# Optimization experiments

Measured on AMD Instinct MI355X. Metric: run time of the kernel, lower is better.

Reference implementation:

```python
import jax, jax.numpy as jnp
import numpy as np

FACTOR = 1.0

def _dct_matrix():
    n = 8
    D = np.zeros((n * n, n * n), dtype=np.float32)
    for u in range(n):
        for v in range(n):
            au = 1.0 / np.sqrt(2.0) if u == 0 else 1.0
            av = 1.0 / np.sqrt(2.0) if v == 0 else 1.0
            alpha = au * av * 0.25
            for x in range(n):
                for y in range(n):
                    D[u * n + v, x * n + y] = alpha * np.cos((2 * x + 1) * u * np.pi / 16) * np.cos((2 * y + 1) * v * np.pi / 16)
    return D

def _y_quant_table():
    t = np.array([[16, 11, 10, 16, 24, 40, 51, 61], [12, 12, 14, 19, 26, 58, 60, 55],
                  [14, 13, 16, 24, 40, 57, 69, 56], [14, 17, 22, 29, 51, 87, 80, 62],
                  [18, 22, 37, 56, 68, 109, 103, 77], [24, 35, 55, 64, 81, 104, 113, 92],
                  [49, 64, 78, 87, 103, 121, 120, 101], [72, 92, 95, 98, 112, 100, 103, 99]],
                 dtype=np.float32).T
    return t

def _c_quant_table():
    t = np.full((8, 8), 99, dtype=np.float32)
    t[:4, :4] = np.array([[17, 18, 24, 47], [18, 21, 26, 66], [24, 26, 56, 99], [47, 66, 99, 99]],
                          dtype=np.float32).T
    return t

_D = jnp.asarray(_dct_matrix())          # [64,64]
_QT = jnp.stack([jnp.asarray(_y_quant_table()),
                 jnp.asarray(_c_quant_table()),
                 jnp.asarray(_c_quant_table())], axis=0) * FACTOR  # [3,8,8]

def setup_inputs() -> dict:
    key = jax.random.key(0)
    image = jax.random.uniform(key, (32, 3, 512, 512), dtype=jnp.float32)
    return {"image": image}

def _diffjpeg(image):
    x = jnp.clip(image, 0.0, 1.0)
    B, C, H, W = x.shape  # H, W multiples of 8 -> no padding branch
    r, g, b = x[:, 0], x[:, 1], x[:, 2]
    y = 0.299 * r + 0.587 * g + 0.114 * b
    cb = (b - y) * 0.564 + 0.5
    cr = (r - y) * 0.713 + 0.5
    ycbcr = jnp.stack([y, cb, cr], axis=1)  # [B,3,H,W]
    # blockify into 8x8 tiles
    nh, nw = H // 8, W // 8
    blocks = ycbcr.reshape(B, C, nh, 8, nw, 8).transpose(0, 1, 2, 4, 3, 5)  # [B,C,nh,nw,8,8]
    flat = blocks.reshape(-1, 64) * 255.0 - 128.0
    dct = flat @ _D.T                      # matmul(D, flat.T).T
    dctb = dct.reshape(B, C, nh, nw, 8, 8)
    qte = _QT[None, :, None, None, :, :]   # [1,3,1,1,8,8]
    q = dctb / qte
    q = q + jax.lax.stop_gradient(jnp.round(q) - q)  # STE rounding
    deq = q * qte
    idct = deq.reshape(-1, 64) @ _D        # matmul(D.T, x.T).T
    idct = (idct + 128.0) / 255.0
    img = idct.reshape(B, C, nh, nw, 8, 8).transpose(0, 1, 2, 4, 3, 5).reshape(B, C, H, W)
    yy, ycb, ycr = img[:, 0], img[:, 1] - 0.5, img[:, 2] - 0.5
    rr = yy + 1.403 * ycr
    gg = yy - 0.714 * ycr - 0.344 * ycb
    bb = yy + 1.773 * ycb
    rgb = jnp.clip(jnp.stack([rr, gg, bb], axis=1), 0.0, 1.0)
    return jnp.clip(rgb, 0.0, 1.0)

def reference(image):
    return _diffjpeg(image)
```

## Files before the change

### kernel.cpp

```cpp
#include <hip/hip_runtime.h>

typedef float f32x2 __attribute__((ext_vector_type(2)));

#define K4 0.353553391f
#define K1 0.490392640f
#define K3 0.415734806f
#define K5 0.277785117f
#define K7 0.097545161f
#define K2 0.461939766f
#define K6 0.191341716f

__device__ __align__(16) const float YQT[64] = {
    16.f, 12.f, 14.f, 14.f,  18.f,  24.f,  49.f,  72.f,
    11.f, 12.f, 13.f, 17.f,  22.f,  35.f,  64.f,  92.f,
    10.f, 14.f, 16.f, 22.f,  37.f,  55.f,  78.f,  95.f,
    16.f, 19.f, 24.f, 29.f,  56.f,  64.f,  87.f,  98.f,
    24.f, 26.f, 40.f, 51.f,  68.f,  81.f, 103.f, 112.f,
    40.f, 58.f, 57.f, 87.f, 109.f, 104.f, 121.f, 100.f,
    51.f, 60.f, 69.f, 80.f, 103.f, 113.f, 120.f, 103.f,
    61.f, 55.f, 56.f, 62.f,  77.f,  92.f, 101.f,  99.f
};
__device__ __align__(16) const float RYQT[64] = {
    1.f/16.f, 1.f/12.f, 1.f/14.f, 1.f/14.f, 1.f/18.f,  1.f/24.f,  1.f/49.f,  1.f/72.f,
    1.f/11.f, 1.f/12.f, 1.f/13.f, 1.f/17.f, 1.f/22.f,  1.f/35.f,  1.f/64.f,  1.f/92.f,
    1.f/10.f, 1.f/14.f, 1.f/16.f, 1.f/22.f, 1.f/37.f,  1.f/55.f,  1.f/78.f,  1.f/95.f,
    1.f/16.f, 1.f/19.f, 1.f/24.f, 1.f/29.f, 1.f/56.f,  1.f/64.f,  1.f/87.f,  1.f/98.f,
    1.f/24.f, 1.f/26.f, 1.f/40.f, 1.f/51.f, 1.f/68.f,  1.f/81.f,  1.f/103.f, 1.f/112.f,
    1.f/40.f, 1.f/58.f, 1.f/57.f, 1.f/87.f, 1.f/109.f, 1.f/104.f, 1.f/121.f, 1.f/100.f,
    1.f/51.f, 1.f/60.f, 1.f/69.f, 1.f/80.f, 1.f/103.f, 1.f/113.f, 1.f/120.f, 1.f/103.f,
    1.f/61.f, 1.f/55.f, 1.f/56.f, 1.f/62.f, 1.f/77.f,  1.f/92.f,  1.f/101.f, 1.f/99.f
};
__device__ __align__(16) const float CQ[64] = {
    17.f, 18.f, 24.f, 47.f, 99.f, 99.f, 99.f, 99.f,
    18.f, 21.f, 26.f, 66.f, 99.f, 99.f, 99.f, 99.f,
    24.f, 26.f, 56.f, 99.f, 99.f, 99.f, 99.f, 99.f,
    47.f, 66.f, 99.f, 99.f, 99.f, 99.f, 99.f, 99.f,
    99.f, 99.f, 99.f, 99.f, 99.f, 99.f, 99.f, 99.f,
    99.f, 99.f, 99.f, 99.f, 99.f, 99.f, 99.f, 99.f,
    99.f, 99.f, 99.f, 99.f, 99.f, 99.f, 99.f, 99.f,
    99.f, 99.f, 99.f, 99.f, 99.f, 99.f, 99.f, 99.f
};
__device__ __align__(16) const float RCQ[64] = {
    1.f/17.f, 1.f/18.f, 1.f/24.f, 1.f/47.f, 1.f/99.f, 1.f/99.f, 1.f/99.f, 1.f/99.f,
    1.f/18.f, 1.f/21.f, 1.f/26.f, 1.f/66.f, 1.f/99.f, 1.f/99.f, 1.f/99.f, 1.f/99.f,
    1.f/24.f, 1.f/26.f, 1.f/56.f, 1.f/99.f, 1.f/99.f, 1.f/99.f, 1.f/99.f, 1.f/99.f,
    1.f/47.f, 1.f/66.f, 1.f/99.f, 1.f/99.f, 1.f/99.f, 1.f/99.f, 1.f/99.f, 1.f/99.f,
    1.f/99.f, 1.f/99.f, 1.f/99.f, 1.f/99.f, 1.f/99.f, 1.f/99.f, 1.f/99.f, 1.f/99.f,
    1.f/99.f, 1.f/99.f, 1.f/99.f, 1.f/99.f, 1.f/99.f, 1.f/99.f, 1.f/99.f, 1.f/99.f,
    1.f/99.f, 1.f/99.f, 1.f/99.f, 1.f/99.f, 1.f/99.f, 1.f/99.f, 1.f/99.f, 1.f/99.f,
    1.f/99.f, 1.f/99.f, 1.f/99.f, 1.f/99.f, 1.f/99.f, 1.f/99.f, 1.f/99.f, 1.f/99.f
};

__device__ __forceinline__ float gfma(float a, float b, float c) { return fmaf(a, b, c); }
__device__ __forceinline__ f32x2 gfma(f32x2 a, f32x2 b, f32x2 c) { return __builtin_elementwise_fma(a, b, c); }
__device__ __forceinline__ f32x2 gfma(float a, f32x2 b, f32x2 c) { return __builtin_elementwise_fma((f32x2){a, a}, b, c); }

__device__ __forceinline__ float clamp01(float x) { return __builtin_amdgcn_fmed3f(x, 0.f, 1.f); }

template <typename T>
__device__ __forceinline__ void dct8(const T x[8], T X[8]) {
    const T a0 = x[0] + x[7], a1 = x[1] + x[6], a2 = x[2] + x[5], a3 = x[3] + x[4];
    const T d0 = x[0] - x[7], d1 = x[1] - x[6], d2 = x[2] - x[5], d3 = x[3] - x[4];
    const T e0 = a0 + a3, e1 = a1 + a2, f0 = a0 - a3, f1 = a1 - a2;
    X[0] = K4 * (e0 + e1);
    X[4] = K4 * (e0 - e1);
    X[2] = gfma(K6, f1, K2 * f0);
    X[6] = gfma(-K2, f1, K6 * f0);
    X[1] = gfma(K7, d3, gfma(K5, d2, gfma(K3, d1, K1 * d0)));
    X[3] = gfma(-K5, d3, gfma(-K1, d2, gfma(-K7, d1, K3 * d0)));
    X[5] = gfma(K3, d3, gfma(K7, d2, gfma(-K1, d1, K5 * d0)));
    X[7] = gfma(-K1, d3, gfma(K3, d2, gfma(-K5, d1, K7 * d0)));
}

template <typename T>
__device__ __forceinline__ void idct8(const T X[8], T x[8]) {
    const T g0 = K4 * (X[0] + X[4]);
    const T g1 = K4 * (X[0] - X[4]);
    const T E0 = gfma(K6, X[6], gfma(K2, X[2], g0));
    const T E1 = gfma(-K2, X[6], gfma(K6, X[2], g1));
    const T E2 = gfma(K2, X[6], gfma(-K6, X[2], g1));
    const T E3 = gfma(-K6, X[6], gfma(-K2, X[2], g0));
    const T O0 = gfma(K7, X[7], gfma(K5, X[5], gfma(K3, X[3], K1 * X[1])));
    const T O1 = gfma(-K5, X[7], gfma(-K1, X[5], gfma(-K7, X[3], K3 * X[1])));
    const T O2 = gfma(K3, X[7], gfma(K7, X[5], gfma(-K1, X[3], K5 * X[1])));
    const T O3 = gfma(-K1, X[7], gfma(K3, X[5], gfma(-K5, X[3], K7 * X[1])));
    x[0] = E0 + O0;  x[7] = E0 - O0;
    x[1] = E1 + O1;  x[6] = E1 - O1;
    x[2] = E2 + O2;  x[5] = E2 - O2;
    x[3] = E3 + O3;  x[4] = E3 - O3;
}

__device__ __forceinline__ f32x2 quant2(f32x2 sv, f32x2 qt, f32x2 rq) {
    const f32x2 q0 = sv * rq;
    const f32x2 e  = gfma(-qt, q0, sv);
    const f32x2 q  = gfma(rq, e, q0);
    const f32x2 n  = {rintf(q.x), rintf(q.y)};
    return n * qt;
}

__device__ __forceinline__ void wave_lds_fence() {
    asm volatile("s_waitcnt lgkmcnt(0)" ::: "memory");
}

#define LDSW 68

__global__ __launch_bounds__(256, 4) void diffjpeg_kernel(const float* __restrict__ in,
                                                          float* __restrict__ out)
{
    __shared__ __align__(16) float pl[3][32][LDSW];

    const int t  = threadIdx.x;
    const int l  = t & 63;
    const int wv = t >> 6;
    const int r0 = wv * 8;

    const int bid  = blockIdx.x;
    const int img  = bid >> 5;
    const int rem  = bid & 31;
    const int band = rem >> 3;
    const int tcol = rem & 7;
    const size_t HW = (size_t)512 * 512;
    const size_t sbase = (size_t)img * 3 * HW + (size_t)(band * 128 + wv * 8) * 512 + (size_t)(tcol * 64);
    const float* __restrict__ pin  = in  + sbase + l;
    float* __restrict__       pout = out + sbase + l;
    const size_t istep = (size_t)32 * 512;

    float rv[8], gv[8], bv[8];
    #pragma unroll
    for (int x = 0; x < 8; ++x) rv[x] = pin[(size_t)x * 512];
    #pragma unroll
    for (int x = 0; x < 8; ++x) gv[x] = pin[HW + (size_t)x * 512];
    #pragma unroll
    for (int x = 0; x < 8; ++x) bv[x] = pin[2 * HW + (size_t)x * 512];

    for (int it = 0; it < 4; ++it) {
        float yv[8];
        f32x2 cc[8];
        #pragma unroll
        for (int x = 0; x < 8; ++x) {
            const float r = clamp01(rv[x]);
            const float g = clamp01(gv[x]);
            const float b = clamp01(bv[x]);
            const float Y = fmaf(76.245f, r, fmaf(149.685f, g, 29.07f * b));
            yv[x] = Y - 128.f;
            const f32x2 tbr = gfma(255.f, (f32x2){b, r}, (f32x2){-Y, -Y});
            cc[x] = gfma((f32x2){0.564f, 0.713f}, tbr, (f32x2){-0.5f, -0.5f});
        }

        if (it < 3) {
            const float* pn = pin + (size_t)(it + 1) * istep;
            #pragma unroll
            for (int x = 0; x < 8; ++x) rv[x] = pn[(size_t)x * 512];
            #pragma unroll
            for (int x = 0; x < 8; ++x) gv[x] = pn[HW + (size_t)x * 512];
            #pragma unroll
            for (int x = 0; x < 8; ++x) bv[x] = pn[2 * HW + (size_t)x * 512];
        }

        {
            float X0[8];
            f32x2 XC[8];
            dct8(yv, X0);
            dct8(cc, XC);
            #pragma unroll
            for (int u = 0; u < 8; ++u) {
                pl[0][r0 + u][l] = X0[u];
                pl[1][r0 + u][l] = XC[u].x;
                pl[2][r0 + u][l] = XC[u].y;
            }
        }
        wave_lds_fence();

        {
            const int b8 = (l >> 3) * 8;
            const int rr = l & 7;

            const float4* yq4  = (const float4*)&YQT[rr * 8];
            const float4* ryq4 = (const float4*)&RYQT[rr * 8];
            const float4* cq4  = (const float4*)&CQ[rr * 8];
            const float4* rcq4 = (const float4*)&RCQ[rr * 8];
            const float4 yqa = yq4[0],  yqb = yq4[1];
            const float4 rya = ryq4[0], ryb = ryq4[1];
            const float4 cqa = cq4[0],  cqb = cq4[1];
            const float4 rca = rcq4[0], rcb4 = rcq4[1];
            const float yq[8]  = {yqa.x, yqa.y, yqa.z, yqa.w, yqb.x, yqb.y, yqb.z, yqb.w};
            const float ryq[8] = {rya.x, rya.y, rya.z, rya.w, ryb.x, ryb.y, ryb.z, ryb.w};
            const float cq[8]  = {cqa.x, cqa.y, cqa.z, cqa.w, cqb.x, cqb.y, cqb.z, cqb.w};
            const float rcq[8] = {rca.x, rca.y, rca.z, rca.w, rcb4.x, rcb4.y, rcb4.z, rcb4.w};

            {
                float4* rp = (float4*)&pl[0][r0 + rr][b8];
                const float4 a0 = rp[0];
                const float4 a1 = rp[1];
                const float T[8] = {a0.x, a0.y, a0.z, a0.w, a1.x, a1.y, a1.z, a1.w};
                float S[8];
                dct8(T, S);
                float Dq[8];
                #pragma unroll
                for (int i = 0; i < 4; ++i) {
                    const f32x2 d = quant2((f32x2){S[2*i], S[2*i+1]},
                                           (f32x2){yq[2*i], yq[2*i+1]},
                                           (f32x2){ryq[2*i], ryq[2*i+1]});
                    Dq[2*i] = d.x; Dq[2*i+1] = d.y;
                }
                float o[8];
                idct8(Dq, o);
                rp[0] = make_float4(o[0], o[1], o[2], o[3]);
                rp[1] = make_float4(o[4], o[5], o[6], o[7]);
            }

            {
                float4* rpb = (float4*)&pl[1][r0 + rr][b8];
                float4* rpr = (float4*)&pl[2][r0 + rr][b8];
                const float4 c0 = rpb[0], c1 = rpb[1];
                const float4 e0 = rpr[0], e1 = rpr[1];
                const f32x2 T[8] = {{c0.x, e0.x}, {c0.y, e0.y}, {c0.z, e0.z}, {c0.w, e0.w},
                                    {c1.x, e1.x}, {c1.y, e1.y}, {c1.z, e1.z}, {c1.w, e1.w}};
                f32x2 S[8];
                dct8(T, S);
                f32x2 Dq[8];
                #pragma unroll
                for (int v = 0; v < 8; ++v)
                    Dq[v] = quant2(S[v], (f32x2){cq[v], cq[v]}, (f32x2){rcq[v], rcq[v]});
                f32x2 o[8];
                idct8(Dq, o);
                rpb[0] = make_float4(o[0].x, o[1].x, o[2].x, o[3].x);
                rpb[1] = make_float4(o[4].x, o[5].x, o[6].x, o[7].x);
                rpr[0] = make_float4(o[0].y, o[1].y, o[2].y, o[3].y);
                rpr[1] = make_float4(o[4].y, o[5].y, o[6].y, o[7].y);
            }
        }
        wave_lds_fence();

        {
            float Xy[8];
            f32x2 Xc[8];
            #pragma unroll
            for (int u = 0; u < 8; ++u) {
                Xy[u] = pl[0][r0 + u][l];
                Xc[u] = (f32x2){pl[1][r0 + u][l], pl[2][r0 + u][l]};
            }
            float sy[8];
            f32x2 sc[8];
            idct8(Xy, sy);
            idct8(Xc, sc);

            float* ob = pout + (size_t)it * istep;
            constexpr float inv255 = 1.0f / 255.0f;
            constexpr float Kr = 0.504711754f;
            constexpr float Kg = 0.499886280f;
            constexpr float Kb = 0.505437240f;
            #pragma unroll
            for (int x = 0; x < 8; ++x) {
                const float scb = sc[x].x;
                const float scr = sc[x].y;
                const f32x2 inner = gfma((f32x2){1.403f, 1.773f}, (f32x2){scr, scb},
                                         (f32x2){sy[x], sy[x]});
                const f32x2 rb = gfma(inv255, inner, (f32x2){Kr, Kb});
                const float gg = fmaf(inv255, fmaf(-0.714f, scr, fmaf(-0.344f, scb, sy[x])), Kg);
                __builtin_nontemporal_store(clamp01(rb.x), ob + (size_t)x * 512);
                __builtin_nontemporal_store(clamp01(gg),   ob + HW + (size_t)x * 512);
                __builtin_nontemporal_store(clamp01(rb.y), ob + 2 * HW + (size_t)x * 512);
            }
        }
    }
}

extern "C" void kernel_launch(void* const* d_in, const int* in_sizes, int n_in,
                              void* d_out, int out_size, void* d_ws, size_t ws_size,
                              hipStream_t stream) {
    const float* in = (const float*)d_in[0];
    float* out = (float*)d_out;
    const int B = in_sizes[0] / (3 * 512 * 512);
    const int grid = B * 32;
    diffjpeg_kernel<<<grid, 256, 0, stream>>>(in, out);
}
```

Before: 36.08 us.

## Drop per-block tile loop, quadruple grid, shrink LDS with per-wave interleaved chroma

Each block now handles a single 32-row tile instead of looping over four tiles with register prefetch, and the grid grows fourfold. LDS shrinks to a per-wave buffer that is reused: luma is processed first, then interleaved Cb/Cr pairs. The launch bound rises to 8 blocks per CU. The aim is higher occupancy and lower register/LDS pressure to hide memory latency, at the cost of losing the explicit software prefetch of the next tile and serializing the luma and chroma stages.

Result: faster. 35.04 us (-2.9%).

```diff
diff --git a/kernel.cpp b/kernel.cpp
--- a/kernel.cpp
+++ b/kernel.cpp
@@ -102,28 +102,32 @@
     asm volatile("s_waitcnt lgkmcnt(0)" ::: "memory");
 }
 
-#define LDSW 68
-
-__global__ __launch_bounds__(256, 4) void diffjpeg_kernel(const float* __restrict__ in,
+#define YW 68
+#define CW 70
+
+__global__ __launch_bounds__(256, 8) void diffjpeg_kernel(const float* __restrict__ in,
                                                           float* __restrict__ out)
 {
-    __shared__ __align__(16) float pl[3][32][LDSW];
+    __shared__ __align__(16) f32x2 lds[4][8][CW];
 
     const int t  = threadIdx.x;
     const int l  = t & 63;
     const int wv = t >> 6;
-    const int r0 = wv * 8;
+    const int b8 = (l >> 3) * 8;
+    const int rr = l & 7;
+
+    f32x2 (*plc)[CW] = lds[wv];
+    float* ply = (float*)&lds[wv][0][0];
 
     const int bid  = blockIdx.x;
-    const int img  = bid >> 5;
-    const int rem  = bid & 31;
-    const int band = rem >> 3;
+    const int img  = bid >> 7;
+    const int rem  = bid & 127;
+    const int trow = rem >> 3;
     const int tcol = rem & 7;
     const size_t HW = (size_t)512 * 512;
-    const size_t sbase = (size_t)img * 3 * HW + (size_t)(band * 128 + wv * 8) * 512 + (size_t)(tcol * 64);
+    const size_t sbase = (size_t)img * 3 * HW + (size_t)(trow * 32 + wv * 8) * 512 + (size_t)(tcol * 64);
     const float* __restrict__ pin  = in  + sbase + l;
     float* __restrict__       pout = out + sbase + l;
-    const size_t istep = (size_t)32 * 512;
 
     float rv[8], gv[8], bv[8];
     #pragma unroll
@@ -133,135 +137,120 @@
     #pragma unroll
     for (int x = 0; x < 8; ++x) bv[x] = pin[2 * HW + (size_t)x * 512];
 
-    for (int it = 0; it < 4; ++it) {
-        float yv[8];
-        f32x2 cc[8];
-        #pragma unroll
-        for (int x = 0; x < 8; ++x) {
-            const float r = clamp01(rv[x]);
-            const float g = clamp01(gv[x]);
-            const float b = clamp01(bv[x]);
-            const float Y = fmaf(76.245f, r, fmaf(149.685f, g, 29.07f * b));
-            yv[x] = Y - 128.f;
-            const f32x2 tbr = gfma(255.f, (f32x2){b, r}, (f32x2){-Y, -Y});
-            cc[x] = gfma((f32x2){0.564f, 0.713f}, tbr, (f32x2){-0.5f, -0.5f});
-        }
-
-        if (it < 3) {
-            const float* pn = pin + (size_t)(it + 1) * istep;
-            #pragma unroll
-            for (int x = 0; x < 8; ++x) rv[x] = pn[(size_t)x * 512];
-            #pragma unroll
-            for (int x = 0; x < 8; ++x) gv[x] = pn[HW + (size_t)x * 512];
-            #pragma unroll
-            for (int x = 0; x < 8; ++x) bv[x] = pn[2 * HW + (size_t)x * 512];
-        }
+    float yv[8];
+    f32x2 cc[8];
+    #pragma unroll
+    for (int x = 0; x < 8; ++x) {
+        const float r = clamp01(rv[x]);
+        const float g = clamp01(gv[x]);
+        const float b = clamp01(bv[x]);
+        const float Y = fmaf(76.245f, r, fmaf(149.685f, g, 29.07f * b));
+        yv[x] = Y - 128.f;
+        const f32x2 tbr = gfma(255.f, (f32x2){b, r}, (f32x2){-Y, -Y});
+        cc[x] = gfma((f32x2){0.564f, 0.713f}, tbr, (f32x2){-0.5f, -0.5f});
+    }
+
+    float sy[8];
+    {
+        float X0[8];
+        dct8(yv, X0);
+        #pragma unroll
+        for (int u = 0; u < 8; ++u) ply[u * YW + l] = X0[u];
+        wave_lds_fence();
 
         {
-            float X0[8];
-            f32x2 XC[8];
-            dct8(yv, X0);
-            dct8(cc, XC);
-            #pragma unroll
-            for (int u = 0; u < 8; ++u) {
-                pl[0][r0 + u][l] = X0[u];
-                pl[1][r0 + u][l] = XC[u].x;
-                pl[2][r0 + u][l] = XC[u].y;
-            }
-        }
-        wave_lds_fence();
-
-        {
-            const int b8 = (l >> 3) * 8;
-            const int rr = l & 7;
-
             const float4* yq4  = (const float4*)&YQT[rr * 8];
             const float4* ryq4 = (const float4*)&RYQT[rr * 8];
+            const float4 yqa = yq4[0],  yqb = yq4[1];
+            const float4 rya = ryq4[0], ryb = ryq4[1];
+            const float yq[8]  = {yqa.x, yqa.y, yqa.z, yqa.w, yqb.x, yqb.y, yqb.z, yqb.w};
+            const float ryq[8] = {rya.x, rya.y, rya.z, rya.w, ryb.x, ryb.y, ryb.z, ryb.w};
+
+            float4* rp = (float4*)(ply + rr * YW + b8);
+            const float4 a0 = rp[0];
+            const float4 a1 = rp[1];
+            const float T[8] = {a0.x, a0.y, a0.z, a0.w, a1.x, a1.y, a1.z, a1.w};
+            float S[8];
+            dct8(T, S);
+            float Dq[8];
+            #pragma unroll
+            for (int i = 0; i < 4; ++i) {
+                const f32x2 d = quant2((f32x2){S[2*i], S[2*i+1]},
+                                       (f32x2){yq[2*i], yq[2*i+1]},
+                                       (f32x2){ryq[2*i], ryq[2*i+1]});
+                Dq[2*i] = d.x; Dq[2*i+1] = d.y;
+            }
+            float o[8];
+            idct8(Dq, o);
+            rp[0] = make_float4(o[0], o[1], o[2], o[3]);
+            rp[1] = make_float4(o[4], o[5], o[6], o[7]);
+        }
+        wave_lds_fence();
+
+        float Xy[8];
+        #pragma unroll
+        for (int u = 0; u < 8; ++u) Xy[u] = ply[u * YW + l];
+        idct8(Xy, sy);
+    }
+    wave_lds_fence();
+
+    f32x2 sc[8];
+    {
+        f32x2 XC[8];
+        dct8(cc, XC);
+        #pragma unroll
+        for (int u = 0; u < 8; ++u) plc[u][l] = XC[u];
+        wave_lds_fence();
+
+        {
             const float4* cq4  = (const float4*)&CQ[rr * 8];
             const float4* rcq4 = (const float4*)&RCQ[rr * 8];
-            const float4 yqa = yq4[0],  yqb = yq4[1];
-            const float4 rya = ryq4[0], ryb = ryq4[1];
             const float4 cqa = cq4[0],  cqb = cq4[1];
             const float4 rca = rcq4[0], rcb4 = rcq4[1];
-            const float yq[8]  = {yqa.x, yqa.y, yqa.z, yqa.w, yqb.x, yqb.y, yqb.z, yqb.w};
-            const float ryq[8] = {rya.x, rya.y, rya.z, rya.w, ryb.x, ryb.y, ryb.z, ryb.w};
             const float cq[8]  = {cqa.x, cqa.y, cqa.z, cqa.w, cqb.x, cqb.y, cqb.z, cqb.w};
             const float rcq[8] = {rca.x, rca.y, rca.z, rca.w, rcb4.x, rcb4.y, rcb4.z, rcb4.w};
 
-            {
-                float4* rp = (float4*)&pl[0][r0 + rr][b8];
-                const float4 a0 = rp[0];
-                const float4 a1 = rp[1];
-                const float T[8] = {a0.x, a0.y, a0.z, a0.w, a1.x, a1.y, a1.z, a1.w};
-                float S[8];
-                dct8(T, S);
-                float Dq[8];
-                #pragma unroll
-                for (int i = 0; i < 4; ++i) {
-                    const f32x2 d = quant2((f32x2){S[2*i], S[2*i+1]},
-                                           (f32x2){yq[2*i], yq[2*i+1]},
-                                           (f32x2){ryq[2*i], ryq[2*i+1]});
-                    Dq[2*i] = d.x; Dq[2*i+1] = d.y;
-                }
-                float o[8];
-                idct8(Dq, o);
-                rp[0] = make_float4(o[0], o[1], o[2], o[3]);
-                rp[1] = make_float4(o[4], o[5], o[6], o[7]);
-            }
-
-            {
-                float4* rpb = (float4*)&pl[1][r0 + rr][b8];
-                float4* rpr = (float4*)&pl[2][r0 + rr][b8];
-                const float4 c0 = rpb[0], c1 = rpb[1];
-                const float4 e0 = rpr[0], e1 = rpr[1];
-                const f32x2 T[8] = {{c0.x, e0.x}, {c0.y, e0.y}, {c0.z, e0.z}, {c0.w, e0.w},
-                                    {c1.x, e1.x}, {c1.y, e1.y}, {c1.z, e1.z}, {c1.w, e1.w}};
-                f32x2 S[8];
-                dct8(T, S);
-                f32x2 Dq[8];
-                #pragma unroll
-                for (int v = 0; v < 8; ++v)
-                    Dq[v] = quant2(S[v], (f32x2){cq[v], cq[v]}, (f32x2){rcq[v], rcq[v]});
-                f32x2 o[8];
-                idct8(Dq, o);
-                rpb[0] = make_float4(o[0].x, o[1].x, o[2].x, o[3].x);
-                rpb[1] = make_float4(o[4].x, o[5].x, o[6].x, o[7].x);
-                rpr[0] = make_float4(o[0].y, o[1].y, o[2].y, o[3].y);
-                rpr[1] = make_float4(o[4].y, o[5].y, o[6].y, o[7].y);
-            }
+            float4* rp = (float4*)&plc[rr][b8];
+            const float4 p0 = rp[0], p1 = rp[1], p2 = rp[2], p3 = rp[3];
+            const f32x2 T[8] = {{p0.x, p0.y}, {p0.z, p0.w}, {p1.x, p1.y}, {p1.z, p1.w},
+                                {p2.x, p2.y}, {p2.z, p2.w}, {p3.x, p3.y}, {p3.z, p3.w}};
+            f32x2 S[8];
+            dct8(T, S);
+            f32x2 Dq[8];
+            #pragma unroll
+            for (int v = 0; v < 8; ++v)
+                Dq[v] = quant2(S[v], (f32x2){cq[v], cq[v]}, (f32x2){rcq[v], rcq[v]});
+            f32x2 o[8];
+            idct8(Dq, o);
+            rp[0] = make_float4(o[0].x, o[0].y, o[1].x, o[1].y);
+            rp[1] = make_float4(o[2].x, o[2].y, o[3].x, o[3].y);
+            rp[2] = make_float4(o[4].x, o[4].y, o[5].x, o[5].y);
+            rp[3] = make_float4(o[6].x, o[6].y, o[7].x, o[7].y);
         }
         wave_lds_fence();
 
-        {
-            float Xy[8];
-            f32x2 Xc[8];
-            #pragma unroll
-            for (int u = 0; u < 8; ++u) {
-                Xy[u] = pl[0][r0 + u][l];
-                Xc[u] = (f32x2){pl[1][r0 + u][l], pl[2][r0 + u][l]};
-            }
-            float sy[8];
-            f32x2 sc[8];
-            idct8(Xy, sy);
-            idct8(Xc, sc);
-
-            float* ob = pout + (size_t)it * istep;
-            constexpr float inv255 = 1.0f / 255.0f;
-            constexpr float Kr = 0.504711754f;
-            constexpr float Kg = 0.499886280f;
-            constexpr float Kb = 0.505437240f;
-            #pragma unroll
-            for (int x = 0; x < 8; ++x) {
-                const float scb = sc[x].x;
-                const float scr = sc[x].y;
-                const f32x2 inner = gfma((f32x2){1.403f, 1.773f}, (f32x2){scr, scb},
-                                         (f32x2){sy[x], sy[x]});
-                const f32x2 rb = gfma(inv255, inner, (f32x2){Kr, Kb});
-                const float gg = fmaf(inv255, fmaf(-0.714f, scr, fmaf(-0.344f, scb, sy[x])), Kg);
-                __builtin_nontemporal_store(clamp01(rb.x), ob + (size_t)x * 512);
-                __builtin_nontemporal_store(clamp01(gg),   ob + HW + (size_t)x * 512);
-                __builtin_nontemporal_store(clamp01(rb.y), ob + 2 * HW + (size_t)x * 512);
-            }
+        f32x2 Xc[8];
+        #pragma unroll
+        for (int u = 0; u < 8; ++u) Xc[u] = plc[u][l];
+        idct8(Xc, sc);
+    }
+
+    {
+        constexpr float inv255 = 1.0f / 255.0f;
+        constexpr float Kr = 0.504711754f;
+        constexpr float Kg = 0.499886280f;
+        constexpr float Kb = 0.505437240f;
+        #pragma unroll
+        for (int x = 0; x < 8; ++x) {
+            const float scb = sc[x].x;
+            const float scr = sc[x].y;
+            const f32x2 inner = gfma((f32x2){1.403f, 1.773f}, (f32x2){scr, scb},
+                                     (f32x2){sy[x], sy[x]});
+            const f32x2 rb = gfma(inv255, inner, (f32x2){Kr, Kb});
+            const float gg = fmaf(inv255, fmaf(-0.714f, scr, fmaf(-0.344f, scb, sy[x])), Kg);
+            __builtin_nontemporal_store(clamp01(rb.x), pout + (size_t)x * 512);
+            __builtin_nontemporal_store(clamp01(gg),   pout + HW + (size_t)x * 512);
+            __builtin_nontemporal_store(clamp01(rb.y), pout + 2 * HW + (size_t)x * 512);
         }
     }
 }
@@ -272,6 +261,6 @@
     const float* in = (const float*)d_in[0];
     float* out = (float*)d_out;
     const int B = in_sizes[0] / (3 * 512 * 512);
-    const int grid = B * 32;
+    const int grid = B * 128;
     diffjpeg_kernel<<<grid, 256, 0, stream>>>(in, out);
 }
```
